# Performance work log

Hardware: AMD Instinct MI355X
Metric: run time of the kernel (lower is better)

Reference implementation:

```python
import jax, jax.numpy as jnp
import numpy as np

B, T, E, H = 4, 1024, 768, 12
HD = E // H                      # 64
R = 2                            # lora rank
LORA_SCALE = 1.0 / R             # loralib default lora_alpha=1 -> alpha/r
NUM_BUCKETS, MAX_DIST = 320, 800


def _rel_bucket(rel):
    nb = NUM_BUCKETS // 2                      # 160
    buckets = (rel > 0).astype(jnp.int32) * nb
    rel = jnp.abs(rel)
    max_exact = nb // 2                        # 80
    is_small = rel < max_exact
    log_ratio = jnp.log(jnp.maximum(rel, 1).astype(jnp.float32) / max_exact)
    large = max_exact + (log_ratio / np.log(MAX_DIST / max_exact) * (nb - max_exact)).astype(jnp.int32)
    large = jnp.minimum(large, nb - 1)
    return buckets + jnp.where(is_small, rel, large)


def setup_inputs() -> dict:
    key = jax.random.key(0)
    ks = jax.random.split(key, 22)
    s = 0.02
    w = lambda k, shape: jax.random.normal(k, shape, jnp.float32) * s
    return {
        "hidden_states": jax.random.normal(ks[0], (B, T, E), jnp.float32),
        "Wq": w(ks[1], (E, E)), "bq": w(ks[2], (E,)),
        "Wk": w(ks[3], (E, E)), "bk": w(ks[4], (E,)),
        "Wv": w(ks[5], (E, E)), "bv": w(ks[6], (E,)),
        "Aq": w(ks[7], (R, E)), "Bq": w(ks[8], (E, R)),
        "Ak": w(ks[9], (R, E)), "Bk": w(ks[10], (E, R)),
        "Av": w(ks[11], (R, E)), "Bv": w(ks[12], (E, R)),
        "Wo": w(ks[13], (E, E)), "bo": w(ks[14], (E,)),
        "Wg": w(ks[15], (8, HD)), "bg": w(ks[16], (8,)),
        "gru_const": jnp.ones((1, H, 1, 1), jnp.float32),
        "rel_embed": w(ks[17], (NUM_BUCKETS, H)),
    }


def reference(hidden_states, Wq, bq, Wk, bk, Wv, bv,
              Aq, Bq, Ak, Bk, Av, Bv, Wo, bo, Wg, bg, gru_const, rel_embed):
    Bsz, Tq, _ = hidden_states.shape
    # --- relative position bias [H, T, T] ---
    pos = jnp.arange(Tq)
    bucket = _rel_bucket(pos[None, :] - pos[:, None])
    pos_bias = rel_embed[bucket].transpose(2, 0, 1)
    # --- dynamic gate from hidden states, per head/position ---
    g = hidden_states.reshape(Bsz, Tq, H, HD).transpose(0, 2, 1, 3)      # [B,H,T,hd]
    gp = jnp.einsum('bhtd,ed->bhte', g, Wg) + bg                          # [B,H,T,8]
    gp = gp.reshape(Bsz, H, Tq, 2, 4).sum(-1)                             # [B,H,T,2]
    gates = jax.nn.sigmoid(gp)
    gate_a, gate_b = gates[..., :1], gates[..., 1:]
    gate = gate_a * (gate_b * gru_const - 1.0) + 2.0                      # [B,H,T,1]
    gated_bias = gate * pos_bias[None]                                    # [B,H,T,T]
    # --- projections: original double-applies q/k/v_proj (proj+LoRA, then
    #     again inside F.multi_head_attention_forward via separate proj weights) ---
    lin = lambda x, W, b: jnp.einsum('bte,oe->bto', x, W) + b
    lora = lambda x, A, Bm: jnp.einsum('bte,re,or->bto', x, A, Bm) * LORA_SCALE
    x = hidden_states
    q1 = lin(x, Wq, bq) + lora(x, Aq, Bq)
    k1 = lin(x, Wk, bk) + lora(x, Ak, Bk)
    v1 = lin(x, Wv, bv) + lora(x, Av, Bv)
    q = lin(q1, Wq, bq) * (HD ** -0.5)
    k = lin(k1, Wk, bk)
    v = lin(v1, Wv, bv)
    qh = q.reshape(Bsz, Tq, H, HD).transpose(0, 2, 1, 3)
    kh = k.reshape(Bsz, Tq, H, HD).transpose(0, 2, 1, 3)
    vh = v.reshape(Bsz, Tq, H, HD).transpose(0, 2, 1, 3)
    scores = jnp.einsum('bhqd,bhkd->bhqk', qh, kh) + gated_bias
    attn = jax.nn.softmax(scores, axis=-1)
    ctx = jnp.einsum('bhqk,bhkd->bhqd', attn, vh)
    out = ctx.transpose(0, 2, 1, 3).reshape(Bsz, Tq, E)
    return jnp.einsum('bte,oe->bto', out, Wo) + bo
```

## Files before the change

### kernel.cpp

```cpp
#include <hip/hip_runtime.h>
#include <math.h>

#define TT 1024
#define EE 768
#define HH 12

typedef __attribute__((ext_vector_type(8))) __bf16 bf16x8;
typedef __attribute__((ext_vector_type(4))) float f32x4;

__device__ __forceinline__ unsigned short f2b(float f) {
    unsigned int u = __float_as_uint(f);
    unsigned int r = (u + 0x7fffu + ((u >> 16) & 1u)) >> 16;
    return (unsigned short)r;
}

#define GLD16(gsrc, ldst) \
    __builtin_amdgcn_global_load_lds( \
        (const __attribute__((address_space(1))) unsigned int*)(gsrc), \
        (__attribute__((address_space(3))) unsigned int*)(ldst), 16, 0, 0)

__global__ __launch_bounds__(256)
void setup_k(const float* __restrict__ hs,
             const float* __restrict__ Wq, const float* __restrict__ Wk,
             const float* __restrict__ Wv, const float* __restrict__ Wo,
             const float* __restrict__ bq, const float* __restrict__ bk,
             const float* __restrict__ bv,
             const float* __restrict__ Aq, const float* __restrict__ Ak,
             const float* __restrict__ Av,
             const float* __restrict__ Bq, const float* __restrict__ Bk,
             const float* __restrict__ Bv,
             const float* __restrict__ Wg, const float* __restrict__ bg,
             const float* __restrict__ gru, const float* __restrict__ rel,
             unsigned short* __restrict__ Wall_b, unsigned short* __restrict__ WT_all,
             float* __restrict__ biasTab, float* __restrict__ bias2,
             float* __restrict__ B2,
             unsigned short* __restrict__ hsb, float* __restrict__ gate,
             float* __restrict__ xA) {
    __shared__ __align__(16) char smem[78080];
    const int bid = blockIdx.x, tid = threadIdx.x;

    if (bid < 1152) {
        size_t base = (size_t)bid * 2048 + tid * 8;
        int mat = (int)(base / 589824);
        size_t local = base % 589824;
        const float* S = mat == 0 ? Wq : (mat == 1 ? Wk : (mat == 2 ? Wv : Wo));
        float4 a = *(const float4*)&S[local];
        float4 c = *(const float4*)&S[local + 4];
        unsigned short hb[8] __attribute__((aligned(16)));
        hb[0] = f2b(a.x); hb[1] = f2b(a.y); hb[2] = f2b(a.z); hb[3] = f2b(a.w);
        hb[4] = f2b(c.x); hb[5] = f2b(c.y); hb[6] = f2b(c.z); hb[7] = f2b(c.w);
        *(uint4*)&Wall_b[base] = *(const uint4*)hb;
    } else if (bid < 1260) {
        unsigned short* Ts = (unsigned short*)smem;
        int v = bid - 1152;
        int mat = v / 36, tile = v % 36;
        int tr = tile / 6, tc = tile % 6;
        const float* S = mat == 0 ? Wq : (mat == 1 ? Wk : Wv);
        #pragma unroll
        for (int i = 0; i < 16; ++i) {
            int idx = i * 256 + tid;
            int row = idx >> 5, col4 = (idx & 31) * 4;
            float4 f = *(const float4*)&S[(size_t)(tr * 128 + row) * EE + tc * 128 + col4];
            Ts[(col4 + 0) * 136 + row] = f2b(f.x);
            Ts[(col4 + 1) * 136 + row] = f2b(f.y);
            Ts[(col4 + 2) * 136 + row] = f2b(f.z);
            Ts[(col4 + 3) * 136 + row] = f2b(f.w);
        }
        __syncthreads();
        unsigned short* dst = WT_all + (size_t)mat * 589824;
        #pragma unroll
        for (int i = 0; i < 8; ++i) {
            int idx = i * 256 + tid;
            int rr = idx >> 4, cg = (idx & 15) * 8;
            *(uint4*)&dst[(size_t)(tc * 128 + rr) * EE + tr * 128 + cg] =
                *(const uint4*)&Ts[rr * 136 + cg];
        }
    } else if (bid < 1356) {
        int idx = (bid - 1260) * 256 + tid;
        if (idx < 2047 * 12) {
            int h = idx % 12;
            int rr = idx / 12;
            int relv = rr - 1023;
            int base = relv > 0 ? 160 : 0;
            int ar = relv < 0 ? -relv : relv;
            int bkt;
            if (ar < 80) bkt = base + ar;
            else {
                double lr = log((double)ar / 80.0);
                int large = 80 + (int)(lr / log(10.0) * 80.0);
                if (large > 159) large = 159;
                bkt = base + large;
            }
            biasTab[h * 2048 + rr] = rel[bkt * 12 + h];
        }
    } else if (bid < 1368) {
        float* bvS = (float*)smem;
        float* BmS = bvS + 768;
        int v = bid - 1356;
        int sel = v / 4, nb = (v % 4) * 192;
        const float* W = sel == 0 ? Wq : (sel == 1 ? Wk : Wv);
        const float* bvec = sel == 0 ? bq : (sel == 1 ? bk : bv);
        const float* Bm = sel == 0 ? Bq : (sel == 1 ? Bk : Bv);
        for (int i = tid; i < 768; i += 256) bvS[i] = bvec[i];
        for (int i = tid; i < 1536; i += 256) BmS[i] = Bm[i];
        __syncthreads();
        if (tid < 192) {
            int n = nb + tid;
            const float* Wrow = W + (size_t)n * EE;
            float a0 = 0.f, a1 = 0.f, a2 = 0.f;
            for (int o = 0; o < EE; o += 4) {
                float4 w = *(const float4*)&Wrow[o];
                a0 += w.x * bvS[o] + w.y * bvS[o + 1] + w.z * bvS[o + 2] + w.w * bvS[o + 3];
                a1 += w.x * BmS[o * 2] + w.y * BmS[o * 2 + 2] + w.z * BmS[o * 2 + 4] + w.w * BmS[o * 2 + 6];
                a2 += w.x * BmS[o * 2 + 1] + w.y * BmS[o * 2 + 3] + w.z * BmS[o * 2 + 5] + w.w * BmS[o * 2 + 7];
            }
            float sc = (sel == 0) ? 0.125f : 1.0f;
            bias2[sel * 768 + n] = (a0 + bvS[n]) * sc;
            B2[sel * 1536 + n * 2 + 0] = a1 * sc;
            B2[sel * 1536 + n * 2 + 1] = a2 * sc;
        }
    } else {
        float* rowF = (float*)smem;
        float* AS   = rowF + 16 * 772;
        float* WgS  = AS + 6 * 768;
        float* gpS  = WgS + 8 * 68;
        float* redS = gpS + 16 * 100;
        float* bgS  = redS + 4 * 96;
        float* gcS  = bgS + 8;
        const int m0 = (bid - 1368) * 16;

        for (int i = tid; i < 512; i += 256) WgS[(i >> 6) * 68 + (i & 63)] = Wg[i];
        for (int i = tid; i < 1152; i += 256) {
            int which = i / 192, c4 = (i % 192) * 4;
            const float* src = (which < 2 ? Aq : (which < 4 ? Ak : Av)) + (which & 1) * 768 + c4;
            float4 f = *(const float4*)src;
            AS[which * 768 + c4 + 0] = f.x; AS[which * 768 + c4 + 1] = f.y;
            AS[which * 768 + c4 + 2] = f.z; AS[which * 768 + c4 + 3] = f.w;
        }
        if (tid < 8)  bgS[tid] = bg[tid];
        if (tid < 12) gcS[tid] = gru[tid];
        #pragma unroll
        for (int i = 0; i < 12; ++i) {
            int idx = i * 256 + tid;
            int row = idx / 192, c4 = (idx % 192) * 4;
            float4 f = *(const float4*)&hs[(size_t)(m0 + row) * EE + c4];
            rowF[row * 772 + c4 + 0] = f.x; rowF[row * 772 + c4 + 1] = f.y;
            rowF[row * 772 + c4 + 2] = f.z; rowF[row * 772 + c4 + 3] = f.w;
            unsigned int lo = (unsigned int)f2b(f.x) | ((unsigned int)f2b(f.y) << 16);
            unsigned int hi = (unsigned int)f2b(f.z) | ((unsigned int)f2b(f.w) << 16);
            uint2 p; p.x = lo; p.y = hi;
            *(uint2*)&hsb[(size_t)(m0 + row) * EE + c4] = p;
        }
        __syncthreads();
        #pragma unroll
        for (int j = 0; j < 6; ++j) {
            int idx = j * 256 + tid;
            int row = idx & 15, q = idx >> 4;
            int h = q % 12, e = q / 12;
            const float* rp = &rowF[row * 772 + h * 64];
            const float* wp = &WgS[e * 68];
            float a = 0.f;
            #pragma unroll 16
            for (int d = 0; d < 64; ++d) a += rp[d] * wp[d];
            gpS[row * 100 + h * 8 + e] = a;
        }
        {
            int row = tid & 15, seg = tid >> 4;
            float s[6] = {0.f, 0.f, 0.f, 0.f, 0.f, 0.f};
            #pragma unroll 8
            for (int j = 0; j < 48; ++j) {
                int e = seg * 48 + j;
                float xv = rowF[row * 772 + e];
                s[0] += xv * AS[e];            s[1] += xv * AS[768 + e];
                s[2] += xv * AS[1536 + e];     s[3] += xv * AS[2304 + e];
                s[4] += xv * AS[3072 + e];     s[5] += xv * AS[3840 + e];
            }
            #pragma unroll
            for (int i = 0; i < 6; ++i) {
                s[i] += __shfl_xor(s[i], 16, 64);
                s[i] += __shfl_xor(s[i], 32, 64);
            }
            int lane = tid & 63, w = tid >> 6;
            if ((lane >> 4) == 0)
                #pragma unroll
                for (int i = 0; i < 6; ++i) redS[w * 96 + row * 6 + i] = s[i];
        }
        __syncthreads();
        if (tid < 96) {
            int row = tid / 6, i = tid % 6;
            float v = redS[row * 6 + i] + redS[96 + row * 6 + i] +
                      redS[192 + row * 6 + i] + redS[288 + row * 6 + i];
            int sel = i >> 1, r = i & 1;
            xA[sel * 8192 + (size_t)(m0 + row) * 2 + r] = v;
        }
        if (tid < 192) {
            int row = tid / 12, h = tid % 12;
            const float* gp = &gpS[row * 100 + h * 8];
            float s0 = gp[0] + gp[1] + gp[2] + gp[3] + bgS[0] + bgS[1] + bgS[2] + bgS[3];
            float s1 = gp[4] + gp[5] + gp[6] + gp[7] + bgS[4] + bgS[5] + bgS[6] + bgS[7];
            float ga = 1.f / (1.f + __expf(-s0));
            float gb = 1.f / (1.f + __expf(-s1));
            int m = m0 + row;
            int b = m >> 10, tp = m & 1023;
            gate[((size_t)b * HH + h) * TT + tp] = ga * (gb * gcS[h] - 1.0f) + 2.0f;
        }
    }
}

__global__ __launch_bounds__(256, 3)
void wgemm_k(const unsigned short* __restrict__ Wall_b,
             const unsigned short* __restrict__ WT_all,
             unsigned short* __restrict__ W2_all) {
    __shared__ unsigned short At[128 * 32];
    __shared__ unsigned short Bt[128 * 32];
    const int tid = threadIdx.x;
    const int bxx = blockIdx.x;
    const int sel = bxx / 36, tile = bxx % 36;
    const int row0 = (tile / 6) * 128, col0 = (tile % 6) * 128;
    const unsigned short* A = Wall_b + (size_t)sel * 589824;
    const unsigned short* Bw = WT_all + (size_t)sel * 589824;

    const int lane = tid & 63, wv = tid >> 6;
    const int wm = (wv & 1) * 64, wn = (wv >> 1) * 64;
    const int l15 = lane & 15, g8 = (lane >> 4) * 8;
    const int lr = lane >> 2, lc = (lane & 3) * 8;
    const int c0 = wv * 2, c1 = wv * 2 + 1;
    const unsigned short* Abase0 = A + (size_t)(row0 + c0 * 16 + lr) * EE + lc;
    const unsigned short* Abase1 = A + (size_t)(row0 + c1 * 16 + lr) * EE + lc;
    const unsigned short* Bbase0 = Bw + (size_t)(col0 + c0 * 16 + lr) * EE + lc;
    const unsigned short* Bbase1 = Bw + (size_t)(col0 + c1 * 16 + lr) * EE + lc;

    f32x4 zero4 = {0.f, 0.f, 0.f, 0.f};
    f32x4 acc[4][4];
    #pragma unroll
    for (int i = 0; i < 4; ++i)
        #pragma unroll
        for (int j = 0; j < 4; ++j) acc[i][j] = zero4;

    for (int kt = 0; kt < 768; kt += 32) {
        GLD16(Abase0 + kt, &At[c0 * 512]);
        GLD16(Abase1 + kt, &At[c1 * 512]);
        GLD16(Bbase0 + kt, &Bt[c0 * 512]);
        GLD16(Bbase1 + kt, &Bt[c1 * 512]);
        __syncthreads();
        bf16x8 af[4], bf[4];
        #pragma unroll
        for (int mt = 0; mt < 4; ++mt) af[mt] = *(const bf16x8*)&At[(wm + mt * 16 + l15) * 32 + g8];
        #pragma unroll
        for (int nt = 0; nt < 4; ++nt) bf[nt] = *(const bf16x8*)&Bt[(wn + nt * 16 + l15) * 32 + g8];
        #pragma unroll
        for (int mt = 0; mt < 4; ++mt)
            #pragma unroll
            for (int nt = 0; nt < 4; ++nt)
                acc[mt][nt] = __builtin_amdgcn_mfma_f32_16x16x32_bf16(af[mt], bf[nt], acc[mt][nt], 0, 0, 0);
        __syncthreads();
    }
    unsigned short* out = W2_all + (size_t)sel * 589824;
    const float sc = (sel == 0) ? 0.125f : 1.0f;
    const int g4 = (lane >> 4) * 4;
    #pragma unroll
    for (int mt = 0; mt < 4; ++mt)
        #pragma unroll
        for (int r = 0; r < 4; ++r) {
            int grow = row0 + wm + mt * 16 + g4 + r;
            #pragma unroll
            for (int nt = 0; nt < 4; ++nt) {
                int ncol = col0 + wn + nt * 16 + l15;
                out[(size_t)grow * EE + ncol] = f2b(acc[mt][nt][r] * sc);
            }
        }
}

__global__ __launch_bounds__(256, 3)
void qkv_gemm_k(const unsigned short* __restrict__ Aall,
                const unsigned short* __restrict__ W2_all,
                const float* __restrict__ bias2,
                const float* __restrict__ xA, const float* __restrict__ B2,
                unsigned short* __restrict__ qb, unsigned short* __restrict__ kb,
                unsigned short* __restrict__ Vtg) {
    __shared__ unsigned short At[128 * 32];
    __shared__ unsigned short Bt[128 * 32];
    __shared__ unsigned short Tv[64 * 136];
    const int tid = threadIdx.x;
    const int bx = blockIdx.x, by = blockIdx.y;
    const int sel = bx / 6;
    const int col0 = (bx % 6) * 128, row0 = by * 128;
    const unsigned short* Wb = W2_all + (size_t)sel * 589824;
    const float* bias = bias2 + sel * 768;

    const int lane = tid & 63, wv = tid >> 6;
    const int wm = (wv & 1) * 64, wn = (wv >> 1) * 64;
    const int l15 = lane & 15, g8 = (lane >> 4) * 8;
    const int lr = lane >> 2, lc = (lane & 3) * 8;
    const int c0 = wv * 2, c1 = wv * 2 + 1;
    const unsigned short* Abase0 = Aall + (size_t)(row0 + c0 * 16 + lr) * EE + lc;
    const unsigned short* Abase1 = Aall + (size_t)(row0 + c1 * 16 + lr) * EE + lc;
    const unsigned short* Bbase0 = Wb + (size_t)(col0 + c0 * 16 + lr) * EE + lc;
    const unsigned short* Bbase1 = Wb + (size_t)(col0 + c1 * 16 + lr) * EE + lc;

    f32x4 zero4 = {0.f, 0.f, 0.f, 0.f};
    f32x4 acc[4][4];
    #pragma unroll
    for (int i = 0; i < 4; ++i)
        #pragma unroll
        for (int j = 0; j < 4; ++j) acc[i][j] = zero4;

    for (int kt = 0; kt < 768; kt += 32) {
        GLD16(Abase0 + kt, &At[c0 * 512]);
        GLD16(Abase1 + kt, &At[c1 * 512]);
        GLD16(Bbase0 + kt, &Bt[c0 * 512]);
        GLD16(Bbase1 + kt, &Bt[c1 * 512]);
        __syncthreads();
        bf16x8 af[4], bf[4];
        #pragma unroll
        for (int mt = 0; mt < 4; ++mt) af[mt] = *(const bf16x8*)&At[(wm + mt * 16 + l15) * 32 + g8];
        #pragma unroll
        for (int nt = 0; nt < 4; ++nt) bf[nt] = *(const bf16x8*)&Bt[(wn + nt * 16 + l15) * 32 + g8];
        #pragma unroll
        for (int mt = 0; mt < 4; ++mt)
            #pragma unroll
            for (int nt = 0; nt < 4; ++nt)
                acc[mt][nt] = __builtin_amdgcn_mfma_f32_16x16x32_bf16(af[mt], bf[nt], acc[mt][nt], 0, 0, 0);
        __syncthreads();
    }

    const float* Lbase = xA + sel * 8192;
    const float* B2s   = B2 + sel * 1536;
    const int g4 = (lane >> 4) * 4;
    if (sel < 2) {
        unsigned short* dst = sel == 0 ? qb : kb;
        #pragma unroll
        for (int mt = 0; mt < 4; ++mt) {
            #pragma unroll
            for (int r = 0; r < 4; ++r) {
                size_t grow = (size_t)row0 + wm + mt * 16 + g4 + r;
                float l0 = Lbase[grow * 2], l1 = Lbase[grow * 2 + 1];
                #pragma unroll
                for (int nt = 0; nt < 4; ++nt) {
                    int ncol = col0 + wn + nt * 16 + l15;
                    float c = acc[mt][nt][r] + bias[ncol]
                              + 0.5f * (l0 * B2s[ncol * 2] + l1 * B2s[ncol * 2 + 1]);
                    dst[grow * EE + ncol] = f2b(c);
                }
            }
        }
    } else {
        const int b = row0 >> 10, t0 = row0 & 1023;
        #pragma unroll
        for (int p = 0; p < 2; ++p) {
            __syncthreads();
            if ((wv >> 1) == p) {
                #pragma unroll
                for (int mt = 0; mt < 4; ++mt) {
                    #pragma unroll
                    for (int r = 0; r < 4; ++r) {
                        int rloc = wm + mt * 16 + g4 + r;
                        size_t grow = (size_t)row0 + rloc;
                        float l0 = Lbase[grow * 2], l1 = Lbase[grow * 2 + 1];
                        #pragma unroll
                        for (int nt = 0; nt < 4; ++nt) {
                            int c = nt * 16 + l15;
                            int ncol = col0 + p * 64 + c;
                            float cv = acc[mt][nt][r] + bias[ncol]
                                     + 0.5f * (l0 * B2s[ncol * 2] + l1 * B2s[ncol * 2 + 1]);
                            Tv[c * 136 + rloc] = f2b(cv);
                        }
                    }
                }
            }
            __syncthreads();
            int c = tid >> 2, s = (tid & 3) * 32;
            int colg = col0 + p * 64 + c;
            int h = colg >> 6, d = colg & 63;
            unsigned short* vp = Vtg + (((size_t)b * HH + h) * 64 + d) * TT + t0 + s;
            #pragma unroll
            for (int j = 0; j < 4; ++j)
                *(uint4*)(vp + j * 8) = *(const uint4*)&Tv[c * 136 + s + j * 8];
        }
    }
}

__global__ __launch_bounds__(256, 4)
void attn_k(const unsigned short* __restrict__ qb, const unsigned short* __restrict__ kb,
            const unsigned short* __restrict__ Vtg, const float* __restrict__ gate,
            const float* __restrict__ biasTab, unsigned short* __restrict__ ctx) {
    __shared__ unsigned short Qs[64 * 72];
    __shared__ unsigned short Ks[64 * 72];
    __shared__ unsigned short Vt[64 * 72];
    __shared__ unsigned short Ps[64 * 72];
    const int tid = threadIdx.x;
    const int qt = blockIdx.x, h = blockIdx.y, b = blockIdx.z;

    const int srow = tid >> 2, scol = (tid & 3) * 16;
    {
        const unsigned short* qp = qb + ((size_t)(b * TT + qt * 64 + srow)) * EE + h * 64 + scol;
        *(uint4*)&Qs[srow * 72 + scol]     = *(const uint4*)qp;
        *(uint4*)&Qs[srow * 72 + scol + 8] = *(const uint4*)(qp + 8);
    }
    const int lane = tid & 63, wv = tid >> 6;
    const int m0 = wv * 16;
    const int l15 = lane & 15, g = lane >> 4;

    float li[4];
    f32x4 zero4 = {0.f, 0.f, 0.f, 0.f};
    f32x4 oa[4];
    #pragma unroll
    for (int r = 0; r < 4; ++r) li[r] = 0.f;
    #pragma unroll
    for (int nt = 0; nt < 4; ++nt) oa[nt] = zero4;
    float gv[4];
    #pragma unroll
    for (int r = 0; r < 4; ++r)
        gv[r] = gate[((size_t)(b * HH + h)) * TT + qt * 64 + m0 + 4 * g + r];

    const unsigned short* kpbase = kb + ((size_t)(b * TT + srow)) * EE + h * 64 + scol;
    const unsigned short* vpbase = Vtg + ((size_t)(b * HH + h) * 64 + srow) * TT + scol;
    const float* btab = biasTab + h * 2048 + 1023 + l15 - qt * 64 - m0 - 4 * g;

    uint4 kr0 = *(const uint4*)kpbase;
    uint4 kr1 = *(const uint4*)(kpbase + 8);
    uint4 vr0 = *(const uint4*)vpbase;
    uint4 vr1 = *(const uint4*)(vpbase + 8);

    for (int kt = 0; kt < 16; ++kt) {
        __syncthreads();
        *(uint4*)&Ks[srow * 72 + scol]     = kr0;
        *(uint4*)&Ks[srow * 72 + scol + 8] = kr1;
        *(uint4*)&Vt[srow * 72 + scol]     = vr0;
        *(uint4*)&Vt[srow * 72 + scol + 8] = vr1;
        __syncthreads();
        if (kt < 15) {
            const unsigned short* kp = kpbase + (size_t)(kt + 1) * 64 * EE;
            kr0 = *(const uint4*)kp;
            kr1 = *(const uint4*)(kp + 8);
            const unsigned short* vp = vpbase + (kt + 1) * 64;
            vr0 = *(const uint4*)vp;
            vr1 = *(const uint4*)(vp + 8);
        }
        f32x4 sa[4];
        #pragma unroll
        for (int nt = 0; nt < 4; ++nt) sa[nt] = zero4;
        bf16x8 aq0 = *(const bf16x8*)&Qs[(m0 + l15) * 72 + g * 8];
        bf16x8 aq1 = *(const bf16x8*)&Qs[(m0 + l15) * 72 + 32 + g * 8];
        #pragma unroll
        for (int nt = 0; nt < 4; ++nt) {
            bf16x8 bk0 = *(const bf16x8*)&Ks[(nt * 16 + l15) * 72 + g * 8];
            bf16x8 bk1 = *(const bf16x8*)&Ks[(nt * 16 + l15) * 72 + 32 + g * 8];
            sa[nt] = __builtin_amdgcn_mfma_f32_16x16x32_bf16(aq0, bk0, sa[nt], 0, 0, 0);
            sa[nt] = __builtin_amdgcn_mfma_f32_16x16x32_bf16(aq1, bk1, sa[nt], 0, 0, 0);
        }
        #pragma unroll
        for (int nt = 0; nt < 4; ++nt) {
            const float* bt = btab + kt * 64 + nt * 16;
            #pragma unroll
            for (int r = 0; r < 4; ++r) {
                float e = __expf(fmaf(gv[r], bt[-r], sa[nt][r]));
                li[r] += e;
                Ps[(m0 + 4 * g + r) * 72 + nt * 16 + l15] = f2b(e);
            }
        }
        bf16x8 ap0 = *(const bf16x8*)&Ps[(m0 + l15) * 72 + g * 8];
        bf16x8 ap1 = *(const bf16x8*)&Ps[(m0 + l15) * 72 + 32 + g * 8];
        #pragma unroll
        for (int nt = 0; nt < 4; ++nt) {
            bf16x8 bv0 = *(const bf16x8*)&Vt[(nt * 16 + l15) * 72 + g * 8];
            bf16x8 bv1 = *(const bf16x8*)&Vt[(nt * 16 + l15) * 72 + 32 + g * 8];
            oa[nt] = __builtin_amdgcn_mfma_f32_16x16x32_bf16(ap0, bv0, oa[nt], 0, 0, 0);
            oa[nt] = __builtin_amdgcn_mfma_f32_16x16x32_bf16(ap1, bv1, oa[nt], 0, 0, 0);
        }
    }
    __syncthreads();
    #pragma unroll
    for (int r = 0; r < 4; ++r) {
        #pragma unroll
        for (int msk = 1; msk < 16; msk <<= 1)
            li[r] += __shfl_xor(li[r], msk, 16);
    }
    #pragma unroll
    for (int nt = 0; nt < 4; ++nt)
        #pragma unroll
        for (int r = 0; r < 4; ++r)
            Ks[(m0 + 4 * g + r) * 72 + nt * 16 + l15] = f2b(oa[nt][r] / li[r]);
    __syncthreads();
    {
        unsigned short* cp = ctx + ((size_t)(b * TT + qt * 64 + srow)) * EE + h * 64 + scol;
        *(uint4*)cp       = *(const uint4*)&Ks[srow * 72 + scol];
        *(uint4*)(cp + 8) = *(const uint4*)&Ks[srow * 72 + scol + 8];
    }
}

__global__ __launch_bounds__(256, 4)
void out_gemm_k(const unsigned short* __restrict__ Aall,
                const unsigned short* __restrict__ Wob,
                const float* __restrict__ bo, float* __restrict__ outf) {
    __shared__ unsigned short At[64 * 32];
    __shared__ unsigned short Bt[128 * 32];
    const int tid = threadIdx.x;
    const int col0 = blockIdx.x * 128, row0 = blockIdx.y * 64;

    const int lane = tid & 63, wv = tid >> 6;
    const int wm = (wv & 1) * 32, wn = (wv >> 1) * 64;
    const int l15 = lane & 15, g8 = (lane >> 4) * 8;
    const int lr = lane >> 2, lc = (lane & 3) * 8;
    const int c0 = wv * 2, c1 = wv * 2 + 1;
    const unsigned short* Abase  = Aall + (size_t)(row0 + wv * 16 + lr) * EE + lc;
    const unsigned short* Bbase0 = Wob + (size_t)(col0 + c0 * 16 + lr) * EE + lc;
    const unsigned short* Bbase1 = Wob + (size_t)(col0 + c1 * 16 + lr) * EE + lc;

    f32x4 zero4 = {0.f, 0.f, 0.f, 0.f};
    f32x4 acc[2][4];
    #pragma unroll
    for (int i = 0; i < 2; ++i)
        #pragma unroll
        for (int j = 0; j < 4; ++j) acc[i][j] = zero4;

    for (int kt = 0; kt < 768; kt += 32) {
        GLD16(Abase + kt, &At[wv * 512]);
        GLD16(Bbase0 + kt, &Bt[c0 * 512]);
        GLD16(Bbase1 + kt, &Bt[c1 * 512]);
        __syncthreads();
        bf16x8 af[2], bf[4];
        #pragma unroll
        for (int mt = 0; mt < 2; ++mt) af[mt] = *(const bf16x8*)&At[(wm + mt * 16 + l15) * 32 + g8];
        #pragma unroll
        for (int nt = 0; nt < 4; ++nt) bf[nt] = *(const bf16x8*)&Bt[(wn + nt * 16 + l15) * 32 + g8];
        #pragma unroll
        for (int mt = 0; mt < 2; ++mt)
            #pragma unroll
            for (int nt = 0; nt < 4; ++nt)
                acc[mt][nt] = __builtin_amdgcn_mfma_f32_16x16x32_bf16(af[mt], bf[nt], acc[mt][nt], 0, 0, 0);
        __syncthreads();
    }
    const int g4 = (lane >> 4) * 4;
    #pragma unroll
    for (int mt = 0; mt < 2; ++mt)
        #pragma unroll
        for (int r = 0; r < 4; ++r) {
            size_t grow = (size_t)row0 + wm + mt * 16 + g4 + r;
            #pragma unroll
            for (int nt = 0; nt < 4; ++nt) {
                int ncol = col0 + wn + nt * 16 + l15;
                outf[grow * EE + ncol] = acc[mt][nt][r] + bo[ncol];
            }
        }
}

extern "C" void kernel_launch(void* const* d_in, const int* in_sizes, int n_in,
                              void* d_out, int out_size, void* d_ws, size_t ws_size,
                              hipStream_t stream) {
    const float* hs  = (const float*)d_in[0];
    const float* Wq  = (const float*)d_in[1];
    const float* bq  = (const float*)d_in[2];
    const float* Wk  = (const float*)d_in[3];
    const float* bk  = (const float*)d_in[4];
    const float* Wv  = (const float*)d_in[5];
    const float* bv  = (const float*)d_in[6];
    const float* Aq  = (const float*)d_in[7];
    const float* Bq  = (const float*)d_in[8];
    const float* Ak  = (const float*)d_in[9];
    const float* Bk  = (const float*)d_in[10];
    const float* Av  = (const float*)d_in[11];
    const float* Bv  = (const float*)d_in[12];
    const float* Wo  = (const float*)d_in[13];
    const float* bo  = (const float*)d_in[14];
    const float* Wg  = (const float*)d_in[15];
    const float* bg  = (const float*)d_in[16];
    const float* gru = (const float*)d_in[17];
    const float* rel = (const float*)d_in[18];

    float* ws = (float*)d_ws;
    float* gate    = ws;
    float* biasTab = gate + 49152;
    float* xA      = biasTab + 24576;
    float* bias2   = xA + 24576;
    float* B2      = bias2 + 2304;
    unsigned short* hsb    = (unsigned short*)(B2 + 4608);
    unsigned short* Wall_b = hsb + 3145728;
    unsigned short* WT_all = Wall_b + 4 * 589824;
    unsigned short* W2_all = WT_all + 3 * 589824;
    unsigned short* qb     = W2_all + 3 * 589824;
    unsigned short* kb     = qb + 3145728;
    unsigned short* Vtg    = kb + 3145728;
    unsigned short* ctxb   = Vtg + 3145728;

    setup_k<<<1624, 256, 0, stream>>>(hs, Wq, Wk, Wv, Wo, bq, bk, bv,
                                      Aq, Ak, Av, Bq, Bk, Bv, Wg, bg, gru, rel,
                                      Wall_b, WT_all, biasTab, bias2, B2,
                                      hsb, gate, xA);
    wgemm_k<<<108, 256, 0, stream>>>(Wall_b, WT_all, W2_all);
    qkv_gemm_k<<<dim3(18, 32), 256, 0, stream>>>(hsb, W2_all, bias2, xA, B2, qb, kb, Vtg);
    attn_k<<<dim3(16, 12, 4), 256, 0, stream>>>(qb, kb, Vtg, gate, biasTab, ctxb);
    out_gemm_k<<<dim3(6, 64), 256, 0, stream>>>(ctxb, Wall_b + 3 * 589824, bo, (float*)d_out);
}
```

Measured before the change: 224.9 us.

## Double attention query tile to 128 rows and keep Q fragments in registers

The attention kernel now processes 128 query rows per block (32 per wave, two MFMA row tiles), so each K/V tile loaded into shared memory is reused for twice as many queries. Q fragments are loaded straight from global memory into registers instead of staging through shared memory. This halves the grid to 384 blocks, which lowers K/V reload traffic but raises register pressure and reduces the number of blocks available to fill the GPU.

```diff
diff --git a/kernel.cpp b/kernel.cpp
--- a/kernel.cpp
+++ b/kernel.cpp
@@ -384,38 +384,45 @@
 void attn_k(const unsigned short* __restrict__ qb, const unsigned short* __restrict__ kb,
             const unsigned short* __restrict__ Vtg, const float* __restrict__ gate,
             const float* __restrict__ biasTab, unsigned short* __restrict__ ctx) {
-    __shared__ unsigned short Qs[64 * 72];
     __shared__ unsigned short Ks[64 * 72];
     __shared__ unsigned short Vt[64 * 72];
-    __shared__ unsigned short Ps[64 * 72];
+    __shared__ unsigned short Ps[128 * 72];
     const int tid = threadIdx.x;
     const int qt = blockIdx.x, h = blockIdx.y, b = blockIdx.z;
+    const int lane = tid & 63, wv = tid >> 6;
+    const int m0 = wv * 32;
+    const int l15 = lane & 15, g = lane >> 4;
+    const int g4 = g * 4;
+
+    bf16x8 aq[2][2];
+    #pragma unroll
+    for (int mt = 0; mt < 2; ++mt) {
+        const unsigned short* qp = qb + ((size_t)(b * TT + qt * 128 + m0 + mt * 16 + l15)) * EE + h * 64;
+        aq[mt][0] = *(const bf16x8*)(qp + g * 8);
+        aq[mt][1] = *(const bf16x8*)(qp + 32 + g * 8);
+    }
+
+    float li[2][4];
+    f32x4 zero4 = {0.f, 0.f, 0.f, 0.f};
+    f32x4 oa[2][4];
+    #pragma unroll
+    for (int mt = 0; mt < 2; ++mt) {
+        #pragma unroll
+        for (int r = 0; r < 4; ++r) li[mt][r] = 0.f;
+        #pragma unroll
+        for (int nt = 0; nt < 4; ++nt) oa[mt][nt] = zero4;
+    }
+    float gv[2][4];
+    #pragma unroll
+    for (int mt = 0; mt < 2; ++mt)
+        #pragma unroll
+        for (int r = 0; r < 4; ++r)
+            gv[mt][r] = gate[((size_t)(b * HH + h)) * TT + qt * 128 + m0 + mt * 16 + g4 + r];
 
     const int srow = tid >> 2, scol = (tid & 3) * 16;
-    {
-        const unsigned short* qp = qb + ((size_t)(b * TT + qt * 64 + srow)) * EE + h * 64 + scol;
-        *(uint4*)&Qs[srow * 72 + scol]     = *(const uint4*)qp;
-        *(uint4*)&Qs[srow * 72 + scol + 8] = *(const uint4*)(qp + 8);
-    }
-    const int lane = tid & 63, wv = tid >> 6;
-    const int m0 = wv * 16;
-    const int l15 = lane & 15, g = lane >> 4;
-
-    float li[4];
-    f32x4 zero4 = {0.f, 0.f, 0.f, 0.f};
-    f32x4 oa[4];
-    #pragma unroll
-    for (int r = 0; r < 4; ++r) li[r] = 0.f;
-    #pragma unroll
-    for (int nt = 0; nt < 4; ++nt) oa[nt] = zero4;
-    float gv[4];
-    #pragma unroll
-    for (int r = 0; r < 4; ++r)
-        gv[r] = gate[((size_t)(b * HH + h)) * TT + qt * 64 + m0 + 4 * g + r];
-
     const unsigned short* kpbase = kb + ((size_t)(b * TT + srow)) * EE + h * 64 + scol;
     const unsigned short* vpbase = Vtg + ((size_t)(b * HH + h) * 64 + srow) * TT + scol;
-    const float* btab = biasTab + h * 2048 + 1023 + l15 - qt * 64 - m0 - 4 * g;
+    const float* btab = biasTab + h * 2048 + 1023 + l15 - qt * 128 - m0 - g4;
 
     uint4 kr0 = *(const uint4*)kpbase;
     uint4 kr1 = *(const uint4*)(kpbase + 8);
@@ -437,55 +444,66 @@
             vr0 = *(const uint4*)vp;
             vr1 = *(const uint4*)(vp + 8);
         }
-        f32x4 sa[4];
-        #pragma unroll
-        for (int nt = 0; nt < 4; ++nt) sa[nt] = zero4;
-        bf16x8 aq0 = *(const bf16x8*)&Qs[(m0 + l15) * 72 + g * 8];
-        bf16x8 aq1 = *(const bf16x8*)&Qs[(m0 + l15) * 72 + 32 + g * 8];
         #pragma unroll
         for (int nt = 0; nt < 4; ++nt) {
             bf16x8 bk0 = *(const bf16x8*)&Ks[(nt * 16 + l15) * 72 + g * 8];
             bf16x8 bk1 = *(const bf16x8*)&Ks[(nt * 16 + l15) * 72 + 32 + g * 8];
-            sa[nt] = __builtin_amdgcn_mfma_f32_16x16x32_bf16(aq0, bk0, sa[nt], 0, 0, 0);
-            sa[nt] = __builtin_amdgcn_mfma_f32_16x16x32_bf16(aq1, bk1, sa[nt], 0, 0, 0);
-        }
-        #pragma unroll
-        for (int nt = 0; nt < 4; ++nt) {
+            f32x4 sa[2];
+            #pragma unroll
+            for (int mt = 0; mt < 2; ++mt) {
+                sa[mt] = __builtin_amdgcn_mfma_f32_16x16x32_bf16(aq[mt][0], bk0, zero4, 0, 0, 0);
+                sa[mt] = __builtin_amdgcn_mfma_f32_16x16x32_bf16(aq[mt][1], bk1, sa[mt], 0, 0, 0);
+            }
             const float* bt = btab + kt * 64 + nt * 16;
             #pragma unroll
-            for (int r = 0; r < 4; ++r) {
-                float e = __expf(fmaf(gv[r], bt[-r], sa[nt][r]));
-                li[r] += e;
-                Ps[(m0 + 4 * g + r) * 72 + nt * 16 + l15] = f2b(e);
-            }
-        }
-        bf16x8 ap0 = *(const bf16x8*)&Ps[(m0 + l15) * 72 + g * 8];
-        bf16x8 ap1 = *(const bf16x8*)&Ps[(m0 + l15) * 72 + 32 + g * 8];
+            for (int mt = 0; mt < 2; ++mt) {
+                #pragma unroll
+                for (int r = 0; r < 4; ++r) {
+                    float e = __expf(fmaf(gv[mt][r], bt[-(mt * 16 + r)], sa[mt][r]));
+                    li[mt][r] += e;
+                    Ps[(m0 + mt * 16 + g4 + r) * 72 + nt * 16 + l15] = f2b(e);
+                }
+            }
+        }
+        bf16x8 ap[2][2];
+        #pragma unroll
+        for (int mt = 0; mt < 2; ++mt) {
+            ap[mt][0] = *(const bf16x8*)&Ps[(m0 + mt * 16 + l15) * 72 + g * 8];
+            ap[mt][1] = *(const bf16x8*)&Ps[(m0 + mt * 16 + l15) * 72 + 32 + g * 8];
+        }
         #pragma unroll
         for (int nt = 0; nt < 4; ++nt) {
             bf16x8 bv0 = *(const bf16x8*)&Vt[(nt * 16 + l15) * 72 + g * 8];
             bf16x8 bv1 = *(const bf16x8*)&Vt[(nt * 16 + l15) * 72 + 32 + g * 8];
-            oa[nt] = __builtin_amdgcn_mfma_f32_16x16x32_bf16(ap0, bv0, oa[nt], 0, 0, 0);
-            oa[nt] = __builtin_amdgcn_mfma_f32_16x16x32_bf16(ap1, bv1, oa[nt], 0, 0, 0);
-        }
-    }
-    __syncthreads();
-    #pragma unroll
-    for (int r = 0; r < 4; ++r) {
-        #pragma unroll
-        for (int msk = 1; msk < 16; msk <<= 1)
-            li[r] += __shfl_xor(li[r], msk, 16);
-    }
-    #pragma unroll
-    for (int nt = 0; nt < 4; ++nt)
-        #pragma unroll
-        for (int r = 0; r < 4; ++r)
-            Ks[(m0 + 4 * g + r) * 72 + nt * 16 + l15] = f2b(oa[nt][r] / li[r]);
+            #pragma unroll
+            for (int mt = 0; mt < 2; ++mt) {
+                oa[mt][nt] = __builtin_amdgcn_mfma_f32_16x16x32_bf16(ap[mt][0], bv0, oa[mt][nt], 0, 0, 0);
+                oa[mt][nt] = __builtin_amdgcn_mfma_f32_16x16x32_bf16(ap[mt][1], bv1, oa[mt][nt], 0, 0, 0);
+            }
+        }
+    }
+    #pragma unroll
+    for (int mt = 0; mt < 2; ++mt)
+        #pragma unroll
+        for (int r = 0; r < 4; ++r) {
+            #pragma unroll
+            for (int msk = 1; msk < 16; msk <<= 1)
+                li[mt][r] += __shfl_xor(li[mt][r], msk, 16);
+        }
+    #pragma unroll
+    for (int mt = 0; mt < 2; ++mt)
+        #pragma unroll
+        for (int nt = 0; nt < 4; ++nt)
+            #pragma unroll
+            for (int r = 0; r < 4; ++r)
+                Ps[(m0 + mt * 16 + g4 + r) * 72 + nt * 16 + l15] = f2b(oa[mt][nt][r] / li[mt][r]);
     __syncthreads();
     {
-        unsigned short* cp = ctx + ((size_t)(b * TT + qt * 64 + srow)) * EE + h * 64 + scol;
-        *(uint4*)cp       = *(const uint4*)&Ks[srow * 72 + scol];
-        *(uint4*)(cp + 8) = *(const uint4*)&Ks[srow * 72 + scol + 8];
+        int srow2 = tid >> 1, scol2 = (tid & 1) * 32;
+        unsigned short* cp = ctx + ((size_t)(b * TT + qt * 128 + srow2)) * EE + h * 64 + scol2;
+        #pragma unroll
+        for (int j = 0; j < 4; ++j)
+            *(uint4*)(cp + j * 8) = *(const uint4*)&Ps[srow2 * 72 + scol2 + j * 8];
     }
 }
 
@@ -589,6 +607,6 @@
                                       hsb, gate, xA);
     wgemm_k<<<108, 256, 0, stream>>>(Wall_b, WT_all, W2_all);
     qkv_gemm_k<<<dim3(18, 32), 256, 0, stream>>>(hsb, W2_all, bias2, xA, B2, qb, kb, Vtg);
-    attn_k<<<dim3(16, 12, 4), 256, 0, stream>>>(qb, kb, Vtg, gate, biasTab, ctxb);
+    attn_k<<<dim3(8, 12, 4), 256, 0, stream>>>(qb, kb, Vtg, gate, biasTab, ctxb);
     out_gemm_k<<<dim3(6, 64), 256, 0, stream>>>(ctxb, Wall_b + 3 * 589824, bo, (float*)d_out);
 }
```

New measurement: 233.9 us. 4.0% more time.
